# Performance work log

Measured on AMD Instinct MI355X. Metric: run time of the kernel, lower is better.

## Reference

```python
import jax, jax.numpy as jnp
import numpy as np

N = 50000      # nodes
E = 1600000    # edges (before self loops)
D = 128        # feature dim (input == hidden == final)
L = 3          # num_layers
EPS = 1e-5     # BatchNorm1d eps
SLOPE = 0.2    # GATConv leaky_relu negative slope


def setup_inputs() -> dict:
    key = jax.random.key(0)
    ks = jax.random.split(key, 5)
    x = jax.random.normal(ks[0], (N, D), jnp.float32)
    edge_index = jax.random.randint(ks[1], (2, E), 0, N)
    W = jax.random.normal(ks[2], (L, D, D), jnp.float32) * 0.1
    a_src = jax.random.normal(ks[3], (L, D), jnp.float32) * 0.1
    a_dst = jax.random.normal(ks[4], (L, D), jnp.float32) * 0.1
    b = jnp.zeros((L, D), jnp.float32)
    return {"x": x, "edge_index": edge_index, "W": W,
            "a_src": a_src, "a_dst": a_dst, "b": b}


def _gat_forward(x, src, dst, W, a_src, a_dst, b):
    z = x
    for l in range(L):
        h = z @ W[l]                                   # [N, D]
        # per-edge attention logits: alpha_src[j] + alpha_dst[i]
        e = jax.nn.leaky_relu((h @ a_src[l])[src] + (h @ a_dst[l])[dst], SLOPE)
        # segment softmax over incoming edges of each destination node
        m = jax.lax.stop_gradient(jax.ops.segment_max(e, dst, num_segments=N))
        p = jnp.exp(e - m[dst])
        s = jax.ops.segment_sum(p, dst, num_segments=N)
        alpha = p / s[dst]                             # [E+N]
        # scatter-aggregate weighted source features, add conv bias
        z = jax.ops.segment_sum(alpha[:, None] * h[src], dst, num_segments=N) + b[l]
        # fresh BatchNorm1d (training mode, weight=1, bias=0, biased var) -> ReLU
        mu = jnp.mean(z, axis=0)
        var = jnp.var(z, axis=0)
        z = jax.nn.relu((z - mu) * jax.lax.rsqrt(var + EPS))
        # dropout(p=0.5): identity in deterministic/eval reference
    return z


def reference(x, edge_index, W, a_src, a_dst, b):
    loops = jnp.arange(N, dtype=edge_index.dtype)
    src = jnp.concatenate([edge_index[0], loops])      # GATConv add_self_loops=True
    dst = jnp.concatenate([edge_index[1], loops])
    return _gat_forward(x, src, dst, W, a_src, a_dst, b)
```

## Files before the change

### kernel.cpp

```cpp
#include <hip/hip_runtime.h>
#include <hip/hip_bf16.h>
#include <math.h>

#define N_NODES 50000
#define N_EDGES 1600000
#define DIM 128
#define EPS 1e-5f
#define SLOPE 0.2f
#define NB_SCAN 196
#define NRANGE 8

typedef __attribute__((ext_vector_type(8))) short bf16x8;
typedef __attribute__((ext_vector_type(4))) float f32x4;

__device__ __forceinline__ float lrelu(float x) { return x > 0.f ? x : SLOPE * x; }

__device__ __forceinline__ unsigned short f2bf(float f) {
    unsigned u = __float_as_uint(f);
    unsigned r = (u + 0x7fffu + ((u >> 16) & 1u)) >> 16;
    return (unsigned short)r;
}

__device__ __forceinline__ float2 ldh2(const unsigned short* p) {
    unsigned u = *(const unsigned*)p;
    float2 r;
    r.x = __uint_as_float(u << 16);
    r.y = __uint_as_float(u & 0xffff0000u);
    return r;
}

__global__ void k_degree(const int* __restrict__ dst, int* __restrict__ deg) {
    int i = blockIdx.x * blockDim.x + threadIdx.x;
    if (i < N_EDGES / 4) {
        int4 d = ((const int4*)dst)[i];
        atomicAdd(&deg[d.x], 1);
        atomicAdd(&deg[d.y], 1);
        atomicAdd(&deg[d.z], 1);
        atomicAdd(&deg[d.w], 1);
    }
}

__global__ void k_scan1(const int* __restrict__ deg, int* __restrict__ partial,
                        int* __restrict__ bsum) {
    __shared__ int s[256];
    int t = threadIdx.x, g = blockIdx.x * 256 + t;
    int v = (g < N_NODES) ? deg[g] : 0;
    s[t] = v;
    __syncthreads();
    for (int off = 1; off < 256; off <<= 1) {
        int x = s[t];
        int y = (t >= off) ? s[t - off] : 0;
        __syncthreads();
        s[t] = x + y;
        __syncthreads();
    }
    if (g < N_NODES) partial[g] = s[t] - v;
    if (t == 255) bsum[blockIdx.x] = s[255];
}

__global__ void k_scan2(const int* __restrict__ bsum, int* __restrict__ boff) {
    __shared__ int s[256];
    int t = threadIdx.x;
    int v = (t < NB_SCAN) ? bsum[t] : 0;
    s[t] = v;
    __syncthreads();
    for (int off = 1; off < 256; off <<= 1) {
        int x = s[t];
        int y = (t >= off) ? s[t - off] : 0;
        __syncthreads();
        s[t] = x + y;
        __syncthreads();
    }
    if (t < NB_SCAN) boff[t] = s[t] - v;
    if (t == 255) boff[NB_SCAN] = s[255];
}

__global__ void k_scan3(const int* __restrict__ partial, const int* __restrict__ boff,
                        int* __restrict__ row_ptr) {
    int g = blockIdx.x * 256 + threadIdx.x;
    if (g < N_NODES) row_ptr[g] = partial[g] + boff[blockIdx.x];
    if (g == 0) row_ptr[N_NODES] = boff[NB_SCAN];
}

__global__ void k_scatter_r(const int* __restrict__ src, const int* __restrict__ dst,
                            const int* __restrict__ row_ptr, int* __restrict__ fill,
                            int* __restrict__ col_src) {
    int range = blockIdx.x & (NRANGE - 1);
    int blk = blockIdx.x >> 3;
    int nblk = gridDim.x >> 3;
    int lo = range * (N_NODES / NRANGE);
    int hi = (range == NRANGE - 1) ? N_NODES : lo + (N_NODES / NRANGE);
    int nq = N_EDGES / 4;
    for (int q = blk * blockDim.x + threadIdx.x; q < nq; q += nblk * blockDim.x) {
        int4 d4 = ((const int4*)dst)[q];
        if (d4.x >= lo && d4.x < hi) {
            int pos = row_ptr[d4.x] + atomicAdd(&fill[d4.x], 1);
            col_src[pos] = src[q * 4 + 0];
        }
        if (d4.y >= lo && d4.y < hi) {
            int pos = row_ptr[d4.y] + atomicAdd(&fill[d4.y], 1);
            col_src[pos] = src[q * 4 + 1];
        }
        if (d4.z >= lo && d4.z < hi) {
            int pos = row_ptr[d4.z] + atomicAdd(&fill[d4.z], 1);
            col_src[pos] = src[q * 4 + 2];
        }
        if (d4.w >= lo && d4.w < hi) {
            int pos = row_ptr[d4.w] + atomicAdd(&fill[d4.w], 1);
            col_src[pos] = src[q * 4 + 3];
        }
    }
}

__global__ void k_prepW(const float* __restrict__ W, unsigned short* __restrict__ Wt) {
    int idx = blockIdx.x * 256 + threadIdx.x;
    int l = idx >> 14;
    int k = (idx >> 7) & 127;
    int c = idx & 127;
    Wt[l * 16384 + c * 128 + k] = f2bf(W[l * 16384 + k * 128 + c]);
}

__global__ void k_castx(const float* __restrict__ X, unsigned short* __restrict__ Zb) {
    int idx = blockIdx.x * blockDim.x + threadIdx.x;
    if (idx >= N_NODES * 16) return;
    size_t base = (size_t)idx * 8;
    float4 a = *(const float4*)&X[base];
    float4 b = *(const float4*)&X[base + 4];
    uint4 o;
    o.x = (unsigned)f2bf(a.x) | ((unsigned)f2bf(a.y) << 16);
    o.y = (unsigned)f2bf(a.z) | ((unsigned)f2bf(a.w) << 16);
    o.z = (unsigned)f2bf(b.x) | ((unsigned)f2bf(b.y) << 16);
    o.w = (unsigned)f2bf(b.z) | ((unsigned)f2bf(b.w) << 16);
    *(uint4*)&Zb[base] = o;
}

__global__ __launch_bounds__(256) void k_gemm_mfma(const unsigned short* __restrict__ Zb,
                                                   const unsigned short* __restrict__ Wt,
                                                   float* __restrict__ H,
                                                   unsigned short* __restrict__ Hb) {
    __shared__ unsigned short Bs[128 * 128];
    int tid = threadIdx.x;
    int lane = tid & 63, wave = tid >> 6;

    {
        int c = tid >> 1, kh = tid & 1;
        const unsigned short* gsrc = &Wt[c * 128 + kh * 64];
#pragma unroll
        for (int ch = 0; ch < 8; ++ch) {
            int byte_off = (c * 256 + kh * 128 + ch * 16) ^ ((c & 7) << 4);
            *(int4*)((char*)Bs + byte_off) = *(const int4*)(gsrc + ch * 8);
        }
    }

    int r0 = blockIdx.x * 128 + wave * 32;
    bf16x8 afr[2][4];
#pragma unroll
    for (int rt = 0; rt < 2; ++rt) {
        int row = r0 + rt * 16 + (lane & 15);
#pragma unroll
        for (int ks = 0; ks < 4; ++ks) {
            int k = ks * 32 + (lane >> 4) * 8;
            if (row < N_NODES)
                afr[rt][ks] = *(const bf16x8*)&Zb[(size_t)row * 128 + k];
            else
                afr[rt][ks] = (bf16x8){0, 0, 0, 0, 0, 0, 0, 0};
        }
    }
    __syncthreads();

    f32x4 acc[2][8];
#pragma unroll
    for (int rt = 0; rt < 2; ++rt)
#pragma unroll
        for (int ct = 0; ct < 8; ++ct) acc[rt][ct] = (f32x4){0.f, 0.f, 0.f, 0.f};

#pragma unroll
    for (int ct = 0; ct < 8; ++ct) {
        int c = ct * 16 + (lane & 15);
#pragma unroll
        for (int ks = 0; ks < 4; ++ks) {
            int k = ks * 32 + (lane >> 4) * 8;
            int byte_off = (c * 256 + k * 2) ^ ((c & 7) << 4);
            bf16x8 bfr = *(const bf16x8*)((char*)Bs + byte_off);
            acc[0][ct] = __builtin_amdgcn_mfma_f32_16x16x32_bf16(afr[0][ks], bfr, acc[0][ct], 0, 0, 0);
            acc[1][ct] = __builtin_amdgcn_mfma_f32_16x16x32_bf16(afr[1][ks], bfr, acc[1][ct], 0, 0, 0);
        }
    }

#pragma unroll
    for (int rt = 0; rt < 2; ++rt)
#pragma unroll
        for (int ct = 0; ct < 8; ++ct) {
            int c = ct * 16 + (lane & 15);
#pragma unroll
            for (int j = 0; j < 4; ++j) {
                int row = r0 + rt * 16 + (lane >> 4) * 4 + j;
                if (row < N_NODES) {
                    float v = acc[rt][ct][j];
                    H[(size_t)row * 128 + c] = v;
                    Hb[(size_t)row * 128 + c] = f2bf(v);
                }
            }
        }
}

__global__ void k_alpha(const float* __restrict__ H, const float* __restrict__ a_src,
                        const float* __restrict__ a_dst, float* __restrict__ as_,
                        float* __restrict__ ad_) {
    int node = blockIdx.x * 4 + (threadIdx.x >> 6);
    int lane = threadIdx.x & 63;
    if (node >= N_NODES) return;
    float2 h = *(const float2*)&H[(size_t)node * 128 + lane * 2];
    float2 s = *(const float2*)&a_src[lane * 2];
    float2 d = *(const float2*)&a_dst[lane * 2];
    float ps = h.x * s.x + h.y * s.y;
    float pd = h.x * d.x + h.y * d.y;
#pragma unroll
    for (int off = 32; off; off >>= 1) {
        ps += __shfl_xor(ps, off);
        pd += __shfl_xor(pd, off);
    }
    if (lane == 0) { as_[node] = ps; ad_[node] = pd; }
}

__global__ void k_aggregate(const int* __restrict__ row_ptr, const int* __restrict__ col_src,
                            const unsigned short* __restrict__ Hb,
                            const float* __restrict__ as_, const float* __restrict__ ad_,
                            const float* __restrict__ bias, float* __restrict__ Zout,
                            float* __restrict__ ebuf) {
    int node = blockIdx.x * 4 + (threadIdx.x >> 6);
    int lane = threadIdx.x & 63;
    if (node >= N_NODES) return;

    int start = row_ptr[node], end = row_ptr[node + 1];
    int deg = end - start;
    float ad_i = ad_[node];
    float eself = lrelu(as_[node] + ad_i);
    float m = eself;
    float2 acc;
    float2 hi = ldh2(&Hb[(size_t)node * 128 + lane * 2]);

    if (deg <= 128) {
        int s0 = 0, s1 = 0;
        float e0 = -INFINITY, e1 = -INFINITY;
        if (start + lane < end) {
            s0 = col_src[start + lane];
            e0 = lrelu(as_[s0] + ad_i);
            m = fmaxf(m, e0);
        }
        if (start + 64 + lane < end) {
            s1 = col_src[start + 64 + lane];
            e1 = lrelu(as_[s1] + ad_i);
            m = fmaxf(m, e1);
        }
#pragma unroll
        for (int off = 32; off; off >>= 1) m = fmaxf(m, __shfl_xor(m, off));
        float w0 = __expf(e0 - m);
        float w1 = __expf(e1 - m);
        float p = w0 + w1;
#pragma unroll
        for (int off = 32; off; off >>= 1) p += __shfl_xor(p, off);
        float pself = __expf(eself - m);
        float inv_s = 1.f / (p + pself);
        w0 *= inv_s;
        w1 *= inv_s;
        float wself = pself * inv_s;
        acc.x = wself * hi.x;
        acc.y = wself * hi.y;

        int jmax = deg < 64 ? deg : 64;
        int j = 0;
        for (; j + 8 <= jmax; j += 8) {
            float w[8]; int sv[8];
#pragma unroll
            for (int q = 0; q < 8; ++q) {
                w[q] = __shfl(w0, j + q);
                sv[q] = __shfl(s0, j + q);
            }
            float2 h[8];
#pragma unroll
            for (int q = 0; q < 8; ++q) h[q] = ldh2(&Hb[(size_t)sv[q] * 128 + lane * 2]);
#pragma unroll
            for (int q = 0; q < 8; ++q) {
                acc.x += w[q] * h[q].x;
                acc.y += w[q] * h[q].y;
            }
        }
        for (; j < jmax; ++j) {
            float w = __shfl(w0, j);
            int sv = __shfl(s0, j);
            float2 hs = ldh2(&Hb[(size_t)sv * 128 + lane * 2]);
            acc.x += w * hs.x;
            acc.y += w * hs.y;
        }
        for (j = 64; j < deg; ++j) {
            float w = __shfl(w1, j - 64);
            int sv = __shfl(s1, j - 64);
            float2 hs = ldh2(&Hb[(size_t)sv * 128 + lane * 2]);
            acc.x += w * hs.x;
            acc.y += w * hs.y;
        }
    } else {
        for (int j = start + lane; j < end; j += 64) {
            int sj = col_src[j];
            float e = lrelu(as_[sj] + ad_i);
            ebuf[j] = e;
            m = fmaxf(m, e);
        }
#pragma unroll
        for (int off = 32; off; off >>= 1) m = fmaxf(m, __shfl_xor(m, off));
        float p = 0.f;
        for (int j = start + lane; j < end; j += 64) p += __expf(ebuf[j] - m);
#pragma unroll
        for (int off = 32; off; off >>= 1) p += __shfl_xor(p, off);
        float pself = __expf(eself - m);
        float inv_s = 1.f / (p + pself);
        float wself = pself * inv_s;
        acc.x = wself * hi.x;
        acc.y = wself * hi.y;
        for (int j = start; j < end; ++j) {
            int sv = col_src[j];
            float w = __expf(ebuf[j] - m) * inv_s;
            float2 hs = ldh2(&Hb[(size_t)sv * 128 + lane * 2]);
            acc.x += w * hs.x;
            acc.y += w * hs.y;
        }
    }

    float2 bv = *(const float2*)&bias[lane * 2];
    float2 o;
    o.x = acc.x + bv.x;
    o.y = acc.y + bv.y;
    *(float2*)&Zout[(size_t)node * 128 + lane * 2] = o;
}

__global__ void k_bnstats(const float* __restrict__ Z, float* __restrict__ part) {
    int c = threadIdx.x;
    float s = 0.f, sq = 0.f;
    for (int i = blockIdx.x; i < N_NODES; i += gridDim.x) {
        float v = Z[(size_t)i * 128 + c];
        s += v;
        sq += v * v;
    }
    part[blockIdx.x * 256 + c] = s;
    part[blockIdx.x * 256 + 128 + c] = sq;
}

__global__ void k_bnfinal(const float* __restrict__ part, float* __restrict__ mu,
                          float* __restrict__ rs) {
    int c = threadIdx.x;
    float s = 0.f, sq = 0.f;
    for (int b = 0; b < 512; ++b) {
        s += part[b * 256 + c];
        sq += part[b * 256 + 128 + c];
    }
    float m = s / (float)N_NODES;
    float var = sq / (float)N_NODES - m * m;
    mu[c] = m;
    rs[c] = rsqrtf(var + EPS);
}

__global__ void k_bnapply2(const float* __restrict__ Zin, const float* __restrict__ mu,
                           const float* __restrict__ rs, float* __restrict__ outf,
                           unsigned short* __restrict__ outb) {
    int idx = blockIdx.x * blockDim.x + threadIdx.x;
    if (idx >= N_NODES * 16) return;
    size_t base = (size_t)idx * 8;
    int c = (int)(base & 127);
    float4 a = *(const float4*)&Zin[base];
    float4 b = *(const float4*)&Zin[base + 4];
    float4 m0 = *(const float4*)&mu[c];
    float4 m1 = *(const float4*)&mu[c + 4];
    float4 r0 = *(const float4*)&rs[c];
    float4 r1 = *(const float4*)&rs[c + 4];
    a.x = fmaxf((a.x - m0.x) * r0.x, 0.f);
    a.y = fmaxf((a.y - m0.y) * r0.y, 0.f);
    a.z = fmaxf((a.z - m0.z) * r0.z, 0.f);
    a.w = fmaxf((a.w - m0.w) * r0.w, 0.f);
    b.x = fmaxf((b.x - m1.x) * r1.x, 0.f);
    b.y = fmaxf((b.y - m1.y) * r1.y, 0.f);
    b.z = fmaxf((b.z - m1.z) * r1.z, 0.f);
    b.w = fmaxf((b.w - m1.w) * r1.w, 0.f);
    if (outf) {
        *(float4*)&outf[base] = a;
        *(float4*)&outf[base + 4] = b;
    }
    if (outb) {
        uint4 o;
        o.x = (unsigned)f2bf(a.x) | ((unsigned)f2bf(a.y) << 16);
        o.y = (unsigned)f2bf(a.z) | ((unsigned)f2bf(a.w) << 16);
        o.z = (unsigned)f2bf(b.x) | ((unsigned)f2bf(b.y) << 16);
        o.w = (unsigned)f2bf(b.z) | ((unsigned)f2bf(b.w) << 16);
        *(uint4*)&outb[base] = o;
    }
}

extern "C" void kernel_launch(void* const* d_in, const int* in_sizes, int n_in,
                              void* d_out, int out_size, void* d_ws, size_t ws_size,
                              hipStream_t stream) {
    const float* x = (const float*)d_in[0];
    const int* ei = (const int*)d_in[1];
    const int* srcp = ei;
    const int* dstp = ei + N_EDGES;
    const float* W = (const float*)d_in[2];
    const float* a_src = (const float*)d_in[3];
    const float* a_dst = (const float*)d_in[4];
    const float* bias = (const float*)d_in[5];
    float* out = (float*)d_out;

    char* ws = (char*)d_ws;
    size_t off = 0;
    auto alloc = [&](size_t bytes) -> void* {
        void* p = ws + off;
        off = (off + bytes + 255) & ~(size_t)255;
        return p;
    };
    int* deg      = (int*)alloc(N_NODES * 4);
    int* fill     = (int*)alloc(N_NODES * 4);
    int* row_ptr  = (int*)alloc((N_NODES + 1) * 4);
    int* col_src  = (int*)alloc(N_EDGES * 4);
    float* ebuf   = (float*)alloc(N_EDGES * 4);
    float* hbuf   = (float*)alloc((size_t)N_NODES * DIM * 4);
    unsigned short* hbf = (unsigned short*)alloc((size_t)N_NODES * DIM * 2);
    float* zbuf   = (float*)alloc((size_t)N_NODES * DIM * 4);
    unsigned short* zb = (unsigned short*)alloc((size_t)N_NODES * DIM * 2);
    unsigned short* wtb = (unsigned short*)alloc(3 * 16384 * 2);
    float* asb    = (float*)alloc(N_NODES * 4);
    float* adb    = (float*)alloc(N_NODES * 4);
    float* part   = (float*)alloc(512 * 256 * 4);
    float* mu     = (float*)alloc(128 * 4);
    float* rsg    = (float*)alloc(128 * 4);
    if (off > ws_size) return;

    int* partial = (int*)ebuf;
    int* bsum    = partial + N_NODES;
    int* boff    = bsum + 256;

    hipMemsetAsync(deg, 0, N_NODES * 4, stream);
    hipMemsetAsync(fill, 0, N_NODES * 4, stream);
    k_degree<<<(N_EDGES / 4 + 255) / 256, 256, 0, stream>>>(dstp, deg);
    k_scan1<<<NB_SCAN, 256, 0, stream>>>(deg, partial, bsum);
    k_scan2<<<1, 256, 0, stream>>>(bsum, boff);
    k_scan3<<<NB_SCAN, 256, 0, stream>>>(partial, boff, row_ptr);
    k_scatter_r<<<NRANGE * 128, 256, 0, stream>>>(srcp, dstp, row_ptr, fill, col_src);
    k_prepW<<<192, 256, 0, stream>>>(W, wtb);
    k_castx<<<(N_NODES * 16 + 255) / 256, 256, 0, stream>>>(x, zb);

    for (int l = 0; l < 3; ++l) {
        k_gemm_mfma<<<(N_NODES + 127) / 128, 256, 0, stream>>>(zb, wtb + l * 16384, hbuf, hbf);
        k_alpha<<<(N_NODES + 3) / 4, 256, 0, stream>>>(hbuf, a_src + l * DIM, a_dst + l * DIM,
                                                       asb, adb);
        k_aggregate<<<(N_NODES + 3) / 4, 256, 0, stream>>>(row_ptr, col_src, hbf, asb, adb,
                                                           bias + l * DIM, zbuf, ebuf);
        k_bnstats<<<512, 128, 0, stream>>>(zbuf, part);
        k_bnfinal<<<1, 128, 0, stream>>>(part, mu, rsg);
        k_bnapply2<<<(N_NODES * 16 + 255) / 256, 256, 0, stream>>>(
            zbuf, mu, rsg, (l == 2) ? out : nullptr, (l < 2) ? zb : nullptr);
    }
}
```

Before: 638.4 us.

## Bucket-partition CSR build and fuse BN-apply, cast and alpha into GEMM

Replaces the degree-atomic, three-pass scan and global-atomic scatter CSR build with a two-level bucket partition: a bucket histogram, staging of (src,dst) pairs per bucket, then a per-bucket local scan and scatter done with LDS atomics. The GEMM now reads fp32 Z directly and applies the previous layer's BN+ReLU and the bf16 cast on load. It also computes the attention logits from the accumulators in registers, which removes the separate castx, alpha and per-layer bnapply kernels and the fp32 H buffer. This adds an 8-byte-per-edge staging pass and extra fp32 reads in the GEMM.

```diff
diff --git a/kernel.cpp b/kernel.cpp
--- a/kernel.cpp
+++ b/kernel.cpp
@@ -7,8 +7,11 @@
 #define DIM 128
 #define EPS 1e-5f
 #define SLOPE 0.2f
-#define NB_SCAN 196
-#define NRANGE 8
+
+#define NBUCK 256
+#define NPB 196
+#define EPB 4096
+#define NBLK_B ((N_EDGES + EPB - 1) / EPB)
 
 typedef __attribute__((ext_vector_type(8))) short bf16x8;
 typedef __attribute__((ext_vector_type(4))) float f32x4;
@@ -29,86 +32,120 @@
     return r;
 }
 
-__global__ void k_degree(const int* __restrict__ dst, int* __restrict__ deg) {
-    int i = blockIdx.x * blockDim.x + threadIdx.x;
-    if (i < N_EDGES / 4) {
-        int4 d = ((const int4*)dst)[i];
-        atomicAdd(&deg[d.x], 1);
-        atomicAdd(&deg[d.y], 1);
-        atomicAdd(&deg[d.z], 1);
-        atomicAdd(&deg[d.w], 1);
-    }
-}
-
-__global__ void k_scan1(const int* __restrict__ deg, int* __restrict__ partial,
-                        int* __restrict__ bsum) {
-    __shared__ int s[256];
-    int t = threadIdx.x, g = blockIdx.x * 256 + t;
-    int v = (g < N_NODES) ? deg[g] : 0;
+__global__ void k_hist(const int* __restrict__ dst, int* __restrict__ bcnt) {
+    __shared__ int h[NBUCK];
+    int tid = threadIdx.x;
+    h[tid] = 0;
+    __syncthreads();
+    int nq = N_EDGES / 4;
+    for (int q = blockIdx.x * 256 + tid; q < nq; q += gridDim.x * 256) {
+        int4 d = ((const int4*)dst)[q];
+        atomicAdd(&h[d.x / NPB], 1);
+        atomicAdd(&h[d.y / NPB], 1);
+        atomicAdd(&h[d.z / NPB], 1);
+        atomicAdd(&h[d.w / NPB], 1);
+    }
+    __syncthreads();
+    if (h[tid]) atomicAdd(&bcnt[tid], h[tid]);
+}
+
+__global__ void k_bscan(const int* __restrict__ bcnt, int* __restrict__ bbase,
+                        int* __restrict__ gtail) {
+    __shared__ int s[NBUCK];
+    int t = threadIdx.x;
+    int v = bcnt[t];
     s[t] = v;
     __syncthreads();
-    for (int off = 1; off < 256; off <<= 1) {
+    for (int off = 1; off < NBUCK; off <<= 1) {
         int x = s[t];
         int y = (t >= off) ? s[t - off] : 0;
         __syncthreads();
         s[t] = x + y;
         __syncthreads();
     }
-    if (g < N_NODES) partial[g] = s[t] - v;
-    if (t == 255) bsum[blockIdx.x] = s[255];
-}
-
-__global__ void k_scan2(const int* __restrict__ bsum, int* __restrict__ boff) {
-    __shared__ int s[256];
-    int t = threadIdx.x;
-    int v = (t < NB_SCAN) ? bsum[t] : 0;
-    s[t] = v;
-    __syncthreads();
-    for (int off = 1; off < 256; off <<= 1) {
-        int x = s[t];
-        int y = (t >= off) ? s[t - off] : 0;
+    bbase[t] = s[t] - v;
+    gtail[t] = s[t] - v;
+    if (t == NBUCK - 1) bbase[NBUCK] = s[NBUCK - 1];
+}
+
+__global__ __launch_bounds__(256) void k_partB(const int* __restrict__ src,
+                                               const int* __restrict__ dst,
+                                               int* __restrict__ gtail,
+                                               uint2* __restrict__ staged) {
+    __shared__ int cnt[NBUCK];
+    __shared__ int bas[NBUCK];
+    int tid = threadIdx.x;
+    cnt[tid] = 0;
+    __syncthreads();
+    int e0 = blockIdx.x * EPB;
+#pragma unroll 4
+    for (int i = 0; i < EPB / 256; ++i) {
+        int e = e0 + i * 256 + tid;
+        if (e < N_EDGES) atomicAdd(&cnt[dst[e] / NPB], 1);
+    }
+    __syncthreads();
+    {
+        int c = cnt[tid];
+        bas[tid] = c ? atomicAdd(&gtail[tid], c) : 0;
+    }
+    __syncthreads();
+    cnt[tid] = 0;
+    __syncthreads();
+#pragma unroll 4
+    for (int i = 0; i < EPB / 256; ++i) {
+        int e = e0 + i * 256 + tid;
+        if (e < N_EDGES) {
+            int d = dst[e], s = src[e];
+            int b = d / NPB;
+            int off = atomicAdd(&cnt[b], 1);
+            staged[bas[b] + off] = make_uint2((unsigned)s, (unsigned)d);
+        }
+    }
+}
+
+__global__ __launch_bounds__(256) void k_partC(const uint2* __restrict__ staged,
+                                               const int* __restrict__ bbase,
+                                               int* __restrict__ row_ptr,
+                                               int* __restrict__ col_src) {
+    __shared__ int cnt[NBUCK];
+    __shared__ int loc[NBUCK];
+    __shared__ int s[NBUCK];
+    int b = blockIdx.x, tid = threadIdx.x;
+    int d0 = b * NPB;
+    int d1 = d0 + NPB;
+    if (d1 > N_NODES) d1 = N_NODES;
+    int nn = d1 - d0;
+    int s0 = bbase[b], s1 = bbase[b + 1];
+
+    cnt[tid] = 0;
+    __syncthreads();
+    for (int e = s0 + tid; e < s1; e += 256) {
+        int d = (int)staged[e].y;
+        atomicAdd(&cnt[d - d0], 1);
+    }
+    __syncthreads();
+    {
+        int v = cnt[tid];
+        s[tid] = v;
         __syncthreads();
-        s[t] = x + y;
-        __syncthreads();
-    }
-    if (t < NB_SCAN) boff[t] = s[t] - v;
-    if (t == 255) boff[NB_SCAN] = s[255];
-}
-
-__global__ void k_scan3(const int* __restrict__ partial, const int* __restrict__ boff,
-                        int* __restrict__ row_ptr) {
-    int g = blockIdx.x * 256 + threadIdx.x;
-    if (g < N_NODES) row_ptr[g] = partial[g] + boff[blockIdx.x];
-    if (g == 0) row_ptr[N_NODES] = boff[NB_SCAN];
-}
-
-__global__ void k_scatter_r(const int* __restrict__ src, const int* __restrict__ dst,
-                            const int* __restrict__ row_ptr, int* __restrict__ fill,
-                            int* __restrict__ col_src) {
-    int range = blockIdx.x & (NRANGE - 1);
-    int blk = blockIdx.x >> 3;
-    int nblk = gridDim.x >> 3;
-    int lo = range * (N_NODES / NRANGE);
-    int hi = (range == NRANGE - 1) ? N_NODES : lo + (N_NODES / NRANGE);
-    int nq = N_EDGES / 4;
-    for (int q = blk * blockDim.x + threadIdx.x; q < nq; q += nblk * blockDim.x) {
-        int4 d4 = ((const int4*)dst)[q];
-        if (d4.x >= lo && d4.x < hi) {
-            int pos = row_ptr[d4.x] + atomicAdd(&fill[d4.x], 1);
-            col_src[pos] = src[q * 4 + 0];
-        }
-        if (d4.y >= lo && d4.y < hi) {
-            int pos = row_ptr[d4.y] + atomicAdd(&fill[d4.y], 1);
-            col_src[pos] = src[q * 4 + 1];
-        }
-        if (d4.z >= lo && d4.z < hi) {
-            int pos = row_ptr[d4.z] + atomicAdd(&fill[d4.z], 1);
-            col_src[pos] = src[q * 4 + 2];
-        }
-        if (d4.w >= lo && d4.w < hi) {
-            int pos = row_ptr[d4.w] + atomicAdd(&fill[d4.w], 1);
-            col_src[pos] = src[q * 4 + 3];
-        }
+        for (int off = 1; off < NBUCK; off <<= 1) {
+            int x = s[tid];
+            int y = (tid >= off) ? s[tid - off] : 0;
+            __syncthreads();
+            s[tid] = x + y;
+            __syncthreads();
+        }
+        loc[tid] = s[tid] - v;
+    }
+    if (tid < nn) row_ptr[d0 + tid] = s0 + loc[tid];
+    if (b == 0 && tid == 0) row_ptr[N_NODES] = N_EDGES;
+    cnt[tid] = 0;
+    __syncthreads();
+    for (int e = s0 + tid; e < s1; e += 256) {
+        uint2 sd = staged[e];
+        int d = (int)sd.y;
+        int pos = s0 + loc[d - d0] + atomicAdd(&cnt[d - d0], 1);
+        col_src[pos] = (int)sd.x;
     }
 }
 
@@ -120,24 +157,15 @@
     Wt[l * 16384 + c * 128 + k] = f2bf(W[l * 16384 + k * 128 + c]);
 }
 
-__global__ void k_castx(const float* __restrict__ X, unsigned short* __restrict__ Zb) {
-    int idx = blockIdx.x * blockDim.x + threadIdx.x;
-    if (idx >= N_NODES * 16) return;
-    size_t base = (size_t)idx * 8;
-    float4 a = *(const float4*)&X[base];
-    float4 b = *(const float4*)&X[base + 4];
-    uint4 o;
-    o.x = (unsigned)f2bf(a.x) | ((unsigned)f2bf(a.y) << 16);
-    o.y = (unsigned)f2bf(a.z) | ((unsigned)f2bf(a.w) << 16);
-    o.z = (unsigned)f2bf(b.x) | ((unsigned)f2bf(b.y) << 16);
-    o.w = (unsigned)f2bf(b.z) | ((unsigned)f2bf(b.w) << 16);
-    *(uint4*)&Zb[base] = o;
-}
-
-__global__ __launch_bounds__(256) void k_gemm_mfma(const unsigned short* __restrict__ Zb,
+__global__ __launch_bounds__(256) void k_gemm_mfma(const float* __restrict__ Z,
                                                    const unsigned short* __restrict__ Wt,
-                                                   float* __restrict__ H,
-                                                   unsigned short* __restrict__ Hb) {
+                                                   unsigned short* __restrict__ Hb,
+                                                   const float* __restrict__ mu,
+                                                   const float* __restrict__ rs,
+                                                   const float* __restrict__ a_src,
+                                                   const float* __restrict__ a_dst,
+                                                   float* __restrict__ as_,
+                                                   float* __restrict__ ad_) {
     __shared__ unsigned short Bs[128 * 128];
     int tid = threadIdx.x;
     int lane = tid & 63, wave = tid >> 6;
@@ -157,14 +185,43 @@
 #pragma unroll
     for (int rt = 0; rt < 2; ++rt) {
         int row = r0 + rt * 16 + (lane & 15);
+        const float* zrow = &Z[(size_t)row * 128];
 #pragma unroll
         for (int ks = 0; ks < 4; ++ks) {
             int k = ks * 32 + (lane >> 4) * 8;
-            if (row < N_NODES)
-                afr[rt][ks] = *(const bf16x8*)&Zb[(size_t)row * 128 + k];
-            else
-                afr[rt][ks] = (bf16x8){0, 0, 0, 0, 0, 0, 0, 0};
-        }
+            bf16x8 fr = (bf16x8){0, 0, 0, 0, 0, 0, 0, 0};
+            if (row < N_NODES) {
+                float4 a = *(const float4*)&zrow[k];
+                float4 b = *(const float4*)&zrow[k + 4];
+                if (mu) {
+                    float4 m0 = *(const float4*)&mu[k];
+                    float4 m1 = *(const float4*)&mu[k + 4];
+                    float4 r0v = *(const float4*)&rs[k];
+                    float4 r1v = *(const float4*)&rs[k + 4];
+                    a.x = fmaxf((a.x - m0.x) * r0v.x, 0.f);
+                    a.y = fmaxf((a.y - m0.y) * r0v.y, 0.f);
+                    a.z = fmaxf((a.z - m0.z) * r0v.z, 0.f);
+                    a.w = fmaxf((a.w - m0.w) * r0v.w, 0.f);
+                    b.x = fmaxf((b.x - m1.x) * r1v.x, 0.f);
+                    b.y = fmaxf((b.y - m1.y) * r1v.y, 0.f);
+                    b.z = fmaxf((b.z - m1.z) * r1v.z, 0.f);
+                    b.w = fmaxf((b.w - m1.w) * r1v.w, 0.f);
+                }
+                fr[0] = (short)f2bf(a.x); fr[1] = (short)f2bf(a.y);
+                fr[2] = (short)f2bf(a.z); fr[3] = (short)f2bf(a.w);
+                fr[4] = (short)f2bf(b.x); fr[5] = (short)f2bf(b.y);
+                fr[6] = (short)f2bf(b.z); fr[7] = (short)f2bf(b.w);
+            }
+            afr[rt][ks] = fr;
+        }
+    }
+
+    float asv[8], adv[8];
+#pragma unroll
+    for (int ct = 0; ct < 8; ++ct) {
+        int c = ct * 16 + (lane & 15);
+        asv[ct] = a_src[c];
+        adv[ct] = a_dst[c];
     }
     __syncthreads();
 
@@ -188,39 +245,37 @@
     }
 
 #pragma unroll
-    for (int rt = 0; rt < 2; ++rt)
+    for (int rt = 0; rt < 2; ++rt) {
 #pragma unroll
         for (int ct = 0; ct < 8; ++ct) {
             int c = ct * 16 + (lane & 15);
 #pragma unroll
             for (int j = 0; j < 4; ++j) {
                 int row = r0 + rt * 16 + (lane >> 4) * 4 + j;
-                if (row < N_NODES) {
-                    float v = acc[rt][ct][j];
-                    H[(size_t)row * 128 + c] = v;
-                    Hb[(size_t)row * 128 + c] = f2bf(v);
-                }
-            }
-        }
-}
-
-__global__ void k_alpha(const float* __restrict__ H, const float* __restrict__ a_src,
-                        const float* __restrict__ a_dst, float* __restrict__ as_,
-                        float* __restrict__ ad_) {
-    int node = blockIdx.x * 4 + (threadIdx.x >> 6);
-    int lane = threadIdx.x & 63;
-    if (node >= N_NODES) return;
-    float2 h = *(const float2*)&H[(size_t)node * 128 + lane * 2];
-    float2 s = *(const float2*)&a_src[lane * 2];
-    float2 d = *(const float2*)&a_dst[lane * 2];
-    float ps = h.x * s.x + h.y * s.y;
-    float pd = h.x * d.x + h.y * d.y;
-#pragma unroll
-    for (int off = 32; off; off >>= 1) {
-        ps += __shfl_xor(ps, off);
-        pd += __shfl_xor(pd, off);
-    }
-    if (lane == 0) { as_[node] = ps; ad_[node] = pd; }
+                if (row < N_NODES) Hb[(size_t)row * 128 + c] = f2bf(acc[rt][ct][j]);
+            }
+        }
+#pragma unroll
+        for (int j = 0; j < 4; ++j) {
+            float ps = 0.f, pd = 0.f;
+#pragma unroll
+            for (int ct = 0; ct < 8; ++ct) {
+                float v = acc[rt][ct][j];
+                ps += v * asv[ct];
+                pd += v * adv[ct];
+            }
+#pragma unroll
+            for (int off = 8; off; off >>= 1) {
+                ps += __shfl_xor(ps, off);
+                pd += __shfl_xor(pd, off);
+            }
+            int row = r0 + rt * 16 + (lane >> 4) * 4 + j;
+            if ((lane & 15) == 0 && row < N_NODES) {
+                as_[row] = ps;
+                ad_[row] = pd;
+            }
+        }
+    }
 }
 
 __global__ void k_aggregate(const int* __restrict__ row_ptr, const int* __restrict__ col_src,
@@ -360,39 +415,19 @@
     rs[c] = rsqrtf(var + EPS);
 }
 
-__global__ void k_bnapply2(const float* __restrict__ Zin, const float* __restrict__ mu,
-                           const float* __restrict__ rs, float* __restrict__ outf,
-                           unsigned short* __restrict__ outb) {
+__global__ void k_bnapply(const float* __restrict__ Zin, const float* __restrict__ mu,
+                          const float* __restrict__ rs, float* __restrict__ Zout) {
     int idx = blockIdx.x * blockDim.x + threadIdx.x;
-    if (idx >= N_NODES * 16) return;
-    size_t base = (size_t)idx * 8;
-    int c = (int)(base & 127);
-    float4 a = *(const float4*)&Zin[base];
-    float4 b = *(const float4*)&Zin[base + 4];
-    float4 m0 = *(const float4*)&mu[c];
-    float4 m1 = *(const float4*)&mu[c + 4];
-    float4 r0 = *(const float4*)&rs[c];
-    float4 r1 = *(const float4*)&rs[c + 4];
-    a.x = fmaxf((a.x - m0.x) * r0.x, 0.f);
-    a.y = fmaxf((a.y - m0.y) * r0.y, 0.f);
-    a.z = fmaxf((a.z - m0.z) * r0.z, 0.f);
-    a.w = fmaxf((a.w - m0.w) * r0.w, 0.f);
-    b.x = fmaxf((b.x - m1.x) * r1.x, 0.f);
-    b.y = fmaxf((b.y - m1.y) * r1.y, 0.f);
-    b.z = fmaxf((b.z - m1.z) * r1.z, 0.f);
-    b.w = fmaxf((b.w - m1.w) * r1.w, 0.f);
-    if (outf) {
-        *(float4*)&outf[base] = a;
-        *(float4*)&outf[base + 4] = b;
-    }
-    if (outb) {
-        uint4 o;
-        o.x = (unsigned)f2bf(a.x) | ((unsigned)f2bf(a.y) << 16);
-        o.y = (unsigned)f2bf(a.z) | ((unsigned)f2bf(a.w) << 16);
-        o.z = (unsigned)f2bf(b.x) | ((unsigned)f2bf(b.y) << 16);
-        o.w = (unsigned)f2bf(b.z) | ((unsigned)f2bf(b.w) << 16);
-        *(uint4*)&outb[base] = o;
-    }
+    if (idx >= N_NODES * 32) return;
+    int c4 = idx & 31;
+    float4 v = ((const float4*)Zin)[idx];
+    float4 m4 = ((const float4*)mu)[c4];
+    float4 r4 = ((const float4*)rs)[c4];
+    v.x = fmaxf((v.x - m4.x) * r4.x, 0.f);
+    v.y = fmaxf((v.y - m4.y) * r4.y, 0.f);
+    v.z = fmaxf((v.z - m4.z) * r4.z, 0.f);
+    v.w = fmaxf((v.w - m4.w) * r4.w, 0.f);
+    ((float4*)Zout)[idx] = v;
 }
 
 extern "C" void kernel_launch(void* const* d_in, const int* in_sizes, int n_in,
@@ -415,15 +450,14 @@
         off = (off + bytes + 255) & ~(size_t)255;
         return p;
     };
-    int* deg      = (int*)alloc(N_NODES * 4);
-    int* fill     = (int*)alloc(N_NODES * 4);
+    int* bcnt     = (int*)alloc(NBUCK * 4);
+    int* bbase    = (int*)alloc((NBUCK + 1) * 4);
+    int* gtail    = (int*)alloc(NBUCK * 4);
     int* row_ptr  = (int*)alloc((N_NODES + 1) * 4);
     int* col_src  = (int*)alloc(N_EDGES * 4);
-    float* ebuf   = (float*)alloc(N_EDGES * 4);
-    float* hbuf   = (float*)alloc((size_t)N_NODES * DIM * 4);
+    uint2* staged = (uint2*)alloc((size_t)N_EDGES * 8);
     unsigned short* hbf = (unsigned short*)alloc((size_t)N_NODES * DIM * 2);
     float* zbuf   = (float*)alloc((size_t)N_NODES * DIM * 4);
-    unsigned short* zb = (unsigned short*)alloc((size_t)N_NODES * DIM * 2);
     unsigned short* wtb = (unsigned short*)alloc(3 * 16384 * 2);
     float* asb    = (float*)alloc(N_NODES * 4);
     float* adb    = (float*)alloc(N_NODES * 4);
@@ -432,29 +466,26 @@
     float* rsg    = (float*)alloc(128 * 4);
     if (off > ws_size) return;
 
-    int* partial = (int*)ebuf;
-    int* bsum    = partial + N_NODES;
-    int* boff    = bsum + 256;
-
-    hipMemsetAsync(deg, 0, N_NODES * 4, stream);
-    hipMemsetAsync(fill, 0, N_NODES * 4, stream);
-    k_degree<<<(N_EDGES / 4 + 255) / 256, 256, 0, stream>>>(dstp, deg);
-    k_scan1<<<NB_SCAN, 256, 0, stream>>>(deg, partial, bsum);
-    k_scan2<<<1, 256, 0, stream>>>(bsum, boff);
-    k_scan3<<<NB_SCAN, 256, 0, stream>>>(partial, boff, row_ptr);
-    k_scatter_r<<<NRANGE * 128, 256, 0, stream>>>(srcp, dstp, row_ptr, fill, col_src);
+    float* ebuf = (float*)staged;
+
+    hipMemsetAsync(bcnt, 0, NBUCK * 4, stream);
+    k_hist<<<256, 256, 0, stream>>>(dstp, bcnt);
+    k_bscan<<<1, NBUCK, 0, stream>>>(bcnt, bbase, gtail);
+    k_partB<<<NBLK_B, 256, 0, stream>>>(srcp, dstp, gtail, staged);
+    k_partC<<<NBUCK, 256, 0, stream>>>(staged, bbase, row_ptr, col_src);
     k_prepW<<<192, 256, 0, stream>>>(W, wtb);
-    k_castx<<<(N_NODES * 16 + 255) / 256, 256, 0, stream>>>(x, zb);
-
+
+    const float* zin = x;
     for (int l = 0; l < 3; ++l) {
-        k_gemm_mfma<<<(N_NODES + 127) / 128, 256, 0, stream>>>(zb, wtb + l * 16384, hbuf, hbf);
-        k_alpha<<<(N_NODES + 3) / 4, 256, 0, stream>>>(hbuf, a_src + l * DIM, a_dst + l * DIM,
-                                                       asb, adb);
+        k_gemm_mfma<<<(N_NODES + 127) / 128, 256, 0, stream>>>(
+            zin, wtb + l * 16384, hbf, (l == 0) ? nullptr : mu, rsg,
+            a_src + l * DIM, a_dst + l * DIM, asb, adb);
         k_aggregate<<<(N_NODES + 3) / 4, 256, 0, stream>>>(row_ptr, col_src, hbf, asb, adb,
                                                            bias + l * DIM, zbuf, ebuf);
         k_bnstats<<<512, 128, 0, stream>>>(zbuf, part);
         k_bnfinal<<<1, 128, 0, stream>>>(part, mu, rsg);
-        k_bnapply2<<<(N_NODES * 16 + 255) / 256, 256, 0, stream>>>(
-            zbuf, mu, rsg, (l == 2) ? out : nullptr, (l < 2) ? zb : nullptr);
-    }
-}
+        if (l == 2)
+            k_bnapply<<<(N_NODES * 32 + 255) / 256, 256, 0, stream>>>(zbuf, mu, rsg, out);
+        zin = zbuf;
+    }
+}
```

Result: faster. 515.0 us (-19.3%).
